# Optimization experiments

Hardware: AMD Instinct MI355X
Metric: run time of the kernel (lower is better)

The kernel has to match this reference:

```python
import jax, jax.numpy as jnp
import numpy as np

IN_FEATURES_LS = (64, 128, 256, 512)
OUT_FEATURES = 1024
MAX_FEAT = max(IN_FEATURES_LS)
N_TOKENS = 65536


def setup_inputs() -> dict:
    key = jax.random.key(0)
    kx, kg, kw, kb = jax.random.split(key, 4)
    x = jax.random.normal(kx, (N_TOKENS, MAX_FEAT), dtype=jnp.float32)
    gidx = jax.random.randint(kg, (N_TOKENS,), 0, len(IN_FEATURES_LS))
    # per-sample declared input size; values are exactly entries of IN_FEATURES_LS
    in_feat_size = jnp.asarray(IN_FEATURES_LS, dtype=jnp.int64 if jax.config.jax_enable_x64 else jnp.int32)[gidx]
    weight = jax.random.normal(kw, (len(IN_FEATURES_LS), OUT_FEATURES, MAX_FEAT), dtype=jnp.float32) * 0.02
    bias = jax.random.normal(kb, (len(IN_FEATURES_LS), OUT_FEATURES), dtype=jnp.float32) * 0.02
    return {"x": x, "in_feat_size": in_feat_size, "weight": weight, "bias": bias}


def reference(x, in_feat_size, weight, bias):
    # mask[g, i] = i < in_features_ls[g]; zero out padded weight columns
    sizes = jnp.asarray(IN_FEATURES_LS, dtype=jnp.int32)
    feat_mask = (jnp.arange(MAX_FEAT)[None, :] < sizes[:, None]).astype(x.dtype)  # [G, max_feat]
    out = jnp.zeros(x.shape[:-1] + (OUT_FEATURES,), dtype=x.dtype)
    for idx, feat_size in enumerate(IN_FEATURES_LS):
        w = weight[idx] * feat_mask[idx][None, :]          # [out, max_feat]
        y = jnp.einsum('oi,ni->no', w, x) + bias[idx]       # [N, out]
        sel = (in_feat_size == feat_size).astype(x.dtype)[..., None]
        out = out + sel * y
    return out
```

## Files before the change

kernel.cpp:

```cpp
#include <hip/hip_runtime.h>
#include <hip/hip_bf16.h>

#define N_TOKENS 65536
#define MAXF 512
#define OUTF 1024
#define NGROUP 4

typedef __attribute__((ext_vector_type(8))) short short8;
typedef __attribute__((ext_vector_type(4))) float floatx4;
typedef unsigned short ushort_t;
typedef unsigned int uint_t;

__device__ __forceinline__ uint_t f2bf(float f) {
    uint_t u = __float_as_uint(f);
    u += 0x7fffu + ((u >> 16) & 1u);
    return u >> 16;
}

#define OFF_BASES  0
#define OFF_BHIST  4096
#define OFF_BSTART 8192
#define OFF_LISTS  16384
#define OFF_XB     (1u<<20)
#define OFF_WB     ((1u<<20) + ((size_t)N_TOKENS*MAXF*2))
#define WS_FULL    (OFF_WB + (size_t)NGROUP*OUTF*MAXF*2)
#define WS_MIN     (OFF_LISTS + (size_t)N_TOKENS*4)

__global__ void hist_kernel(const int* __restrict__ sizes, int* __restrict__ blockHist) {
    __shared__ int h[4][NGROUP];
    int t = threadIdx.x, wave = t >> 6;
    int tok = blockIdx.x * 256 + t;
    int g = __ffs(sizes[tok]) - 7;
    #pragma unroll
    for (int gg = 0; gg < NGROUP; ++gg) {
        unsigned long long m = __ballot(g == gg);
        if ((t & 63) == 0) h[wave][gg] = __popcll(m);
    }
    __syncthreads();
    if (t < NGROUP)
        blockHist[blockIdx.x * NGROUP + t] = h[0][t] + h[1][t] + h[2][t] + h[3][t];
}

__global__ void scan_kernel(const int* __restrict__ blockHist,
                            int* __restrict__ blockStart, int* __restrict__ bases) {
    __shared__ int4 sh[256];
    int t = threadIdx.x;
    int4 v = ((const int4*)blockHist)[t];
    sh[t] = v;
    __syncthreads();
    for (int d = 1; d < 256; d <<= 1) {
        int4 u = sh[t];
        int4 a = make_int4(0, 0, 0, 0);
        if (t >= d) a = sh[t - d];
        __syncthreads();
        u.x += a.x; u.y += a.y; u.z += a.z; u.w += a.w;
        sh[t] = u;
        __syncthreads();
    }
    int4 incl = sh[t];
    int4 tot = sh[255];
    int b0 = 0, b1 = tot.x, b2 = b1 + tot.y, b3 = b2 + tot.z, b4 = b3 + tot.w;
    blockStart[t * 4 + 0] = b0 + incl.x - v.x;
    blockStart[t * 4 + 1] = b1 + incl.y - v.y;
    blockStart[t * 4 + 2] = b2 + incl.z - v.z;
    blockStart[t * 4 + 3] = b3 + incl.w - v.w;
    if (t == 0) {
        bases[0] = b0; bases[1] = b1; bases[2] = b2; bases[3] = b3; bases[4] = b4;
    }
}

__global__ void scatter_kernel(const int* __restrict__ sizes,
                               const int* __restrict__ blockStart,
                               int* __restrict__ lists) {
    __shared__ int wcnt[4][NGROUP];
    int t = threadIdx.x, wave = t >> 6, lane = t & 63;
    int tok = blockIdx.x * 256 + t;
    int g = __ffs(sizes[tok]) - 7;
    int pos = 0;
    #pragma unroll
    for (int gg = 0; gg < NGROUP; ++gg) {
        unsigned long long m = __ballot(g == gg);
        if (g == gg) pos = __popcll(m & ((1ull << lane) - 1ull));
        if (lane == 0) wcnt[wave][gg] = __popcll(m);
    }
    __syncthreads();
    int off = blockStart[blockIdx.x * 4 + g];
    for (int w = 0; w < wave; ++w) off += wcnt[w][g];
    lists[off + pos] = tok;
}

__global__ void convx_kernel(const float* __restrict__ x, const int* __restrict__ bases,
                             const int* __restrict__ lists, ushort_t* __restrict__ xb) {
    int slot = blockIdx.x * 4 + (threadIdx.x >> 6);
    int lane = threadIdx.x & 63;
    int b1 = bases[1], b2 = bases[2], b3 = bases[3];
    int g = (slot >= b3) ? 3 : (slot >= b2) ? 2 : (slot >= b1) ? 1 : 0;
    int K = 64 << g;
    int tok = lists[slot];
    const float2* src = (const float2*)(x + (size_t)tok * MAXF);
    uint_t* dst = (uint_t*)(xb + (size_t)slot * MAXF);
    for (int j = lane; j * 2 < K; j += 64) {
        float2 v = src[j];
        dst[j] = f2bf(v.x) | (f2bf(v.y) << 16);
    }
}

__global__ void convw_kernel(const float* __restrict__ weight, ushort_t* __restrict__ wb) {
    int id = blockIdx.x * 256 + threadIdx.x;
    floatx4 v = ((const floatx4*)weight)[id];
    unsigned long long p = (unsigned long long)f2bf(v[0]) |
                           ((unsigned long long)f2bf(v[1]) << 16) |
                           ((unsigned long long)f2bf(v[2]) << 32) |
                           ((unsigned long long)f2bf(v[3]) << 48);
    ((unsigned long long*)wb)[id] = p;
}

#define GLOAD_LDS16(gptr, lptr)                                                \
    __builtin_amdgcn_global_load_lds(                                          \
        (const __attribute__((address_space(1))) uint_t*)(gptr),               \
        (__attribute__((address_space(3))) uint_t*)(lptr), 16, 0, 0)

__global__ __launch_bounds__(256) void gemm_bf16_kernel(
    const ushort_t* __restrict__ xb, const ushort_t* __restrict__ wb,
    const float* __restrict__ bias, const int* __restrict__ bases,
    const int* __restrict__ lists, float* __restrict__ out) {

    const int g = blockIdx.z;
    const int gbase = bases[g];
    const int count = bases[g + 1] - gbase;
    const int m_base = blockIdx.y * 128;
    if (m_base >= count) return;
    const int n_base = blockIdx.x * 128;
    const int K = 64 << g;
    const int rows = min(128, count - m_base);

    __shared__ ushort_t As[128 * 32];
    __shared__ ushort_t Bs[128 * 32];
    __shared__ int oidx[128];

    const int t = threadIdx.x;
    const int wave = t >> 6, lane = t & 63;
    const int wm = wave >> 1, wn = wave & 1;
    const int quad = lane >> 4, l16 = lane & 15;

    const int rsub = lane >> 2;
    const int ksub = (lane & 3) * 8;

    floatx4 acc[4][4];
    #pragma unroll
    for (int i = 0; i < 4; ++i)
        #pragma unroll
        for (int j = 0; j < 4; ++j) acc[i][j] = (floatx4)(0.0f);

    const ushort_t* wg = wb + (size_t)g * OUTF * MAXF;

    for (int k0 = 0; k0 < K; k0 += 32) {
        #pragma unroll
        for (int j = 0; j < 2; ++j) {
            int br = wave * 32 + j * 16;
            int ga = min(gbase + m_base + br + rsub, N_TOKENS - 1);
            GLOAD_LDS16(xb + (size_t)ga * MAXF + k0 + ksub, &As[br * 32]);
            int gb = n_base + br + rsub;
            GLOAD_LDS16(wg + (size_t)gb * MAXF + k0 + ksub, &Bs[br * 32]);
        }
        __syncthreads();

        short8 af[4], bf[4];
        #pragma unroll
        for (int mi = 0; mi < 4; ++mi)
            af[mi] = *(const short8*)&As[(wm * 64 + mi * 16 + l16) * 32 + quad * 8];
        #pragma unroll
        for (int ni = 0; ni < 4; ++ni)
            bf[ni] = *(const short8*)&Bs[(wn * 64 + ni * 16 + l16) * 32 + quad * 8];

        #pragma unroll
        for (int mi = 0; mi < 4; ++mi)
            #pragma unroll
            for (int ni = 0; ni < 4; ++ni)
                acc[mi][ni] = __builtin_amdgcn_mfma_f32_16x16x32_bf16(
                    af[mi], bf[ni], acc[mi][ni], 0, 0, 0);
        __syncthreads();
    }

    if (t < 128) oidx[t] = (t < rows) ? lists[gbase + m_base + t] : 0;
    __syncthreads();

    #pragma unroll
    for (int ni = 0; ni < 4; ++ni) {
        int col = n_base + wn * 64 + ni * 16 + l16;
        float bv = bias[g * OUTF + col];
        #pragma unroll
        for (int mi = 0; mi < 4; ++mi) {
            int mloc = wm * 64 + mi * 16 + quad * 4;
            #pragma unroll
            for (int r = 0; r < 4; ++r) {
                int m = mloc + r;
                if (m < rows)
                    out[(size_t)oidx[m] * OUTF + col] = acc[mi][ni][r] + bv;
            }
        }
    }
}

__global__ __launch_bounds__(256) void gemm_fp32_kernel(
    const float* __restrict__ x, const float* __restrict__ weight,
    const float* __restrict__ bias, const int* __restrict__ bases,
    const int* __restrict__ lists, float* __restrict__ out) {

    const int g = blockIdx.z;
    const int gbase = bases[g];
    const int count = bases[g + 1] - gbase;
    const int m_base = blockIdx.y * 128;
    if (m_base >= count) return;
    const int n_base = blockIdx.x * 128;
    const int K = 64 << g;
    const int rows = min(128, count - m_base);

    __shared__ ushort_t As[128][40];
    __shared__ ushort_t Bs[128][40];
    __shared__ int idxs[128];

    const int t = threadIdx.x;
    if (t < 128) idxs[t] = (t < rows) ? lists[gbase + m_base + t] : lists[gbase + m_base];
    __syncthreads();

    const int wave = t >> 6, lane = t & 63;
    const int wm = wave >> 1, wn = wave & 1;
    const int quad = lane >> 4, l16 = lane & 15;

    floatx4 acc[4][4];
    #pragma unroll
    for (int i = 0; i < 4; ++i)
        #pragma unroll
        for (int j = 0; j < 4; ++j) acc[i][j] = (floatx4)(0.0f);

    const float* wg = weight + (size_t)g * OUTF * MAXF;

    for (int k0 = 0; k0 < K; k0 += 32) {
        #pragma unroll
        for (int rep = 0; rep < 4; ++rep) {
            int id = t + rep * 256;
            int row = id >> 3;
            int kq = id & 7;
            floatx4 av = *(const floatx4*)(x + (size_t)idxs[row] * MAXF + k0 + kq * 4);
            unsigned long long pa = (unsigned long long)f2bf(av[0]) |
                ((unsigned long long)f2bf(av[1]) << 16) |
                ((unsigned long long)f2bf(av[2]) << 32) |
                ((unsigned long long)f2bf(av[3]) << 48);
            *(unsigned long long*)&As[row][kq * 4] = pa;
            floatx4 bv = *(const floatx4*)(wg + (size_t)(n_base + row) * MAXF + k0 + kq * 4);
            unsigned long long pb = (unsigned long long)f2bf(bv[0]) |
                ((unsigned long long)f2bf(bv[1]) << 16) |
                ((unsigned long long)f2bf(bv[2]) << 32) |
                ((unsigned long long)f2bf(bv[3]) << 48);
            *(unsigned long long*)&Bs[row][kq * 4] = pb;
        }
        __syncthreads();

        short8 af[4], bf[4];
        #pragma unroll
        for (int mi = 0; mi < 4; ++mi)
            af[mi] = *(const short8*)&As[wm * 64 + mi * 16 + l16][quad * 8];
        #pragma unroll
        for (int ni = 0; ni < 4; ++ni)
            bf[ni] = *(const short8*)&Bs[wn * 64 + ni * 16 + l16][quad * 8];
        #pragma unroll
        for (int mi = 0; mi < 4; ++mi)
            #pragma unroll
            for (int ni = 0; ni < 4; ++ni)
                acc[mi][ni] = __builtin_amdgcn_mfma_f32_16x16x32_bf16(
                    af[mi], bf[ni], acc[mi][ni], 0, 0, 0);
        __syncthreads();
    }

    #pragma unroll
    for (int ni = 0; ni < 4; ++ni) {
        int col = n_base + wn * 64 + ni * 16 + l16;
        float bv = bias[g * OUTF + col];
        #pragma unroll
        for (int mi = 0; mi < 4; ++mi) {
            int mloc = wm * 64 + mi * 16 + quad * 4;
            #pragma unroll
            for (int r = 0; r < 4; ++r) {
                int m = mloc + r;
                if (m < rows)
                    out[(size_t)idxs[m] * OUTF + col] = acc[mi][ni][r] + bv;
            }
        }
    }
}

extern "C" void kernel_launch(void* const* d_in, const int* in_sizes, int n_in,
                              void* d_out, int out_size, void* d_ws, size_t ws_size,
                              hipStream_t stream) {
    const float* x      = (const float*)d_in[0];
    const int*   sizes  = (const int*)d_in[1];
    const float* weight = (const float*)d_in[2];
    const float* bias   = (const float*)d_in[3];
    float* out = (float*)d_out;

    char* ws = (char*)d_ws;
    int* bases      = (int*)(ws + OFF_BASES);
    int* blockHist  = (int*)(ws + OFF_BHIST);
    int* blockStart = (int*)(ws + OFF_BSTART);
    int* lists      = (int*)(ws + OFF_LISTS);
    ushort_t* xb    = (ushort_t*)(ws + OFF_XB);
    ushort_t* wb    = (ushort_t*)(ws + OFF_WB);

    hist_kernel<<<N_TOKENS / 256, 256, 0, stream>>>(sizes, blockHist);
    scan_kernel<<<1, 256, 0, stream>>>(blockHist, blockStart, bases);
    scatter_kernel<<<N_TOKENS / 256, 256, 0, stream>>>(sizes, blockStart, lists);

    dim3 grid(OUTF / 128, N_TOKENS / 128, NGROUP);
    if (ws_size >= WS_FULL) {
        convw_kernel<<<(NGROUP * OUTF * MAXF / 4) / 256, 256, 0, stream>>>(weight, wb);
        convx_kernel<<<N_TOKENS / 4, 256, 0, stream>>>(x, bases, lists, xb);
        gemm_bf16_kernel<<<grid, 256, 0, stream>>>(xb, wb, bias, bases, lists, out);
    } else {
        gemm_fp32_kernel<<<grid, 256, 0, stream>>>(x, weight, bias, bases, lists, out);
    }
}
```

Baseline: 488.1 us.

## Pack bf16 operands compactly, use 256x256 double-buffered tiles and flat grid

Converted x and weights are now stored densely with a per-group row stride equal to K instead of MAXF, and the conversion kernels use 8-element vectors with grid-stride loops. The GEMM moves to 512-thread blocks with 256x256 tiles, double-buffered LDS prefetch and a flattened 1D grid that only launches the tiles each group needs. The intent is to cut memory traffic, raise operand reuse, overlap loads with MFMA work and drop the empty blocks from the old 3D grid. In exchange the kernel uses more registers and LDS, bases[4] is read where the old code did not, and the grid size of 1036 is hardcoded.

Result: no change. 484.5 us (-0.7%).

```diff
diff --git a/kernel.cpp b/kernel.cpp
--- a/kernel.cpp
+++ b/kernel.cpp
@@ -25,6 +25,8 @@
 #define OFF_WB     ((1u<<20) + ((size_t)N_TOKENS*MAXF*2))
 #define WS_FULL    (OFF_WB + (size_t)NGROUP*OUTF*MAXF*2)
 #define WS_MIN     (OFF_LISTS + (size_t)N_TOKENS*4)
+
+__constant__ int c_wstart[4] = {0, 65536, 196608, 458752};
 
 __global__ void hist_kernel(const int* __restrict__ sizes, int* __restrict__ blockHist) {
     __shared__ int h[4][NGROUP];
@@ -91,28 +93,55 @@
 
 __global__ void convx_kernel(const float* __restrict__ x, const int* __restrict__ bases,
                              const int* __restrict__ lists, ushort_t* __restrict__ xb) {
-    int slot = blockIdx.x * 4 + (threadIdx.x >> 6);
-    int lane = threadIdx.x & 63;
-    int b1 = bases[1], b2 = bases[2], b3 = bases[3];
-    int g = (slot >= b3) ? 3 : (slot >= b2) ? 2 : (slot >= b1) ? 1 : 0;
-    int K = 64 << g;
-    int tok = lists[slot];
-    const float2* src = (const float2*)(x + (size_t)tok * MAXF);
-    uint_t* dst = (uint_t*)(xb + (size_t)slot * MAXF);
-    for (int j = lane; j * 2 < K; j += 64) {
-        float2 v = src[j];
-        dst[j] = f2bf(v.x) | (f2bf(v.y) << 16);
+    int c0 = bases[1] - bases[0], c1 = bases[2] - bases[1],
+        c2 = bases[3] - bases[2], c3 = bases[4] - bases[3];
+    int p1 = c0 << 3;
+    int p2 = p1 + (c1 << 4);
+    int p3 = p2 + (c2 << 5);
+    int T  = p3 + (c3 << 6);
+    int xs1 = c0 << 6;
+    int xs2 = xs1 + (c1 << 7);
+    int xs3 = xs2 + (c2 << 8);
+    int stride = gridDim.x * blockDim.x;
+    for (int id = blockIdx.x * blockDim.x + threadIdx.x; id < T; id += stride) {
+        int g, local, base, xs;
+        if (id < p1)      { g = 0; local = id;      base = bases[0]; xs = 0;   }
+        else if (id < p2) { g = 1; local = id - p1; base = bases[1]; xs = xs1; }
+        else if (id < p3) { g = 2; local = id - p2; base = bases[2]; xs = xs2; }
+        else              { g = 3; local = id - p3; base = bases[3]; xs = xs3; }
+        int shift = 3 + g;
+        int sl = local >> shift;
+        int k  = (local - (sl << shift)) << 3;
+        int tok = lists[base + sl];
+        const floatx4* src = (const floatx4*)(x + (size_t)tok * MAXF + k);
+        floatx4 a = src[0], b = src[1];
+        short8 v;
+        v[0] = (short)f2bf(a[0]); v[1] = (short)f2bf(a[1]);
+        v[2] = (short)f2bf(a[2]); v[3] = (short)f2bf(a[3]);
+        v[4] = (short)f2bf(b[0]); v[5] = (short)f2bf(b[1]);
+        v[6] = (short)f2bf(b[2]); v[7] = (short)f2bf(b[3]);
+        *(short8*)(xb + (size_t)xs + ((size_t)sl << (6 + g)) + k) = v;
     }
 }
 
 __global__ void convw_kernel(const float* __restrict__ weight, ushort_t* __restrict__ wb) {
     int id = blockIdx.x * 256 + threadIdx.x;
-    floatx4 v = ((const floatx4*)weight)[id];
-    unsigned long long p = (unsigned long long)f2bf(v[0]) |
-                           ((unsigned long long)f2bf(v[1]) << 16) |
-                           ((unsigned long long)f2bf(v[2]) << 32) |
-                           ((unsigned long long)f2bf(v[3]) << 48);
-    ((unsigned long long*)wb)[id] = p;
+    int g, local, ws;
+    if (id < 8192)       { g = 0; local = id;         ws = 0;      }
+    else if (id < 24576) { g = 1; local = id - 8192;  ws = 65536;  }
+    else if (id < 57344) { g = 2; local = id - 24576; ws = 196608; }
+    else                 { g = 3; local = id - 57344; ws = 458752; }
+    int shift = 3 + g;
+    int row = local >> shift;
+    int k = (local - (row << shift)) << 3;
+    const floatx4* src = (const floatx4*)(weight + (size_t)g * OUTF * MAXF + (size_t)row * MAXF + k);
+    floatx4 a = src[0], b = src[1];
+    short8 v;
+    v[0] = (short)f2bf(a[0]); v[1] = (short)f2bf(a[1]);
+    v[2] = (short)f2bf(a[2]); v[3] = (short)f2bf(a[3]);
+    v[4] = (short)f2bf(b[0]); v[5] = (short)f2bf(b[1]);
+    v[6] = (short)f2bf(b[2]); v[7] = (short)f2bf(b[3]);
+    *(short8*)(wb + ws + ((size_t)row << (6 + g)) + k) = v;
 }
 
 #define GLOAD_LDS16(gptr, lptr)                                                \
@@ -120,8 +149,121 @@
         (const __attribute__((address_space(1))) uint_t*)(gptr),               \
         (__attribute__((address_space(3))) uint_t*)(lptr), 16, 0, 0)
 
-__global__ __launch_bounds__(256) void gemm_bf16_kernel(
+__global__ __launch_bounds__(512, 1) void gemm_bf16_kernel(
     const ushort_t* __restrict__ xb, const ushort_t* __restrict__ wb,
+    const float* __restrict__ bias, const int* __restrict__ bases,
+    const int* __restrict__ lists, float* __restrict__ out) {
+
+    const int c0 = bases[1] - bases[0], c1 = bases[2] - bases[1],
+              c2 = bases[3] - bases[2], c3 = bases[4] - bases[3];
+    const int t0 = ((c0 + 255) >> 8) << 2;
+    const int t1 = ((c1 + 255) >> 8) << 2;
+    const int t2 = ((c2 + 255) >> 8) << 2;
+    const int t3 = ((c3 + 255) >> 8) << 2;
+    const int xs1 = c0 << 6;
+    const int xs2 = xs1 + (c1 << 7);
+    const int xs3 = xs2 + (c2 << 8);
+
+    int id = blockIdx.x;
+    int g, local, count, gbase, xs, wsb;
+    if (id < t0)                { g = 0; local = id;                count = c0; gbase = bases[0]; xs = 0;   wsb = 0;      }
+    else if (id < t0 + t1)      { g = 1; local = id - t0;           count = c1; gbase = bases[1]; xs = xs1; wsb = 65536;  }
+    else if (id < t0 + t1 + t2) { g = 2; local = id - t0 - t1;      count = c2; gbase = bases[2]; xs = xs2; wsb = 196608; }
+    else if (id < t0 + t1 + t2 + t3)
+                                { g = 3; local = id - t0 - t1 - t2; count = c3; gbase = bases[3]; xs = xs3; wsb = 458752; }
+    else return;
+
+    const int mt = local >> 2, nt = local & 3;
+    const int m_base = mt << 8;
+    const int n_base = nt << 8;
+    const int K_log = 6 + g;
+    const int nsteps = 1 << (g + 1);
+    const int rows = min(256, count - m_base);
+
+    __shared__ ushort_t As[2][256 * 32];
+    __shared__ ushort_t Bs[2][256 * 32];
+
+    const int t = threadIdx.x;
+    const int wave = t >> 6, lane = t & 63;
+    const int wm = wave >> 2, wn = wave & 3;
+    const int quad = lane >> 4, l16 = lane & 15;
+    const int rsub = lane >> 2;
+    const int kq   = (lane & 3) * 8;
+
+    const ushort_t* aptr[2];
+    const ushort_t* bptr[2];
+    #pragma unroll
+    for (int j = 0; j < 2; ++j) {
+        int br = wave * 32 + j * 16;
+        int ar = min(m_base + br + rsub, count - 1);
+        aptr[j] = xb + (size_t)xs + ((size_t)ar << K_log) + kq;
+        int nr = n_base + br + rsub;
+        bptr[j] = wb + (size_t)wsb + ((size_t)nr << K_log) + kq;
+    }
+
+    floatx4 acc[8][4];
+    #pragma unroll
+    for (int i = 0; i < 8; ++i)
+        #pragma unroll
+        for (int j = 0; j < 4; ++j) acc[i][j] = (floatx4)(0.0f);
+
+    #pragma unroll
+    for (int j = 0; j < 2; ++j) {
+        int br = wave * 32 + j * 16;
+        GLOAD_LDS16(aptr[j], &As[0][br * 32]);
+        GLOAD_LDS16(bptr[j], &Bs[0][br * 32]);
+    }
+    __syncthreads();
+
+    int buf = 0;
+    for (int s = 0; s < nsteps; ++s) {
+        if (s + 1 < nsteps) {
+            int k0 = (s + 1) << 5;
+            #pragma unroll
+            for (int j = 0; j < 2; ++j) {
+                int br = wave * 32 + j * 16;
+                GLOAD_LDS16(aptr[j] + k0, &As[buf ^ 1][br * 32]);
+                GLOAD_LDS16(bptr[j] + k0, &Bs[buf ^ 1][br * 32]);
+            }
+        }
+        short8 af[8], bf[4];
+        #pragma unroll
+        for (int mi = 0; mi < 8; ++mi)
+            af[mi] = *(const short8*)&As[buf][(wm * 128 + mi * 16 + l16) * 32 + quad * 8];
+        #pragma unroll
+        for (int ni = 0; ni < 4; ++ni)
+            bf[ni] = *(const short8*)&Bs[buf][(wn * 64 + ni * 16 + l16) * 32 + quad * 8];
+        #pragma unroll
+        for (int mi = 0; mi < 8; ++mi)
+            #pragma unroll
+            for (int ni = 0; ni < 4; ++ni)
+                acc[mi][ni] = __builtin_amdgcn_mfma_f32_16x16x32_bf16(
+                    af[mi], bf[ni], acc[mi][ni], 0, 0, 0);
+        __syncthreads();
+        buf ^= 1;
+    }
+
+    #pragma unroll
+    for (int ni = 0; ni < 4; ++ni) {
+        int col = n_base + wn * 64 + ni * 16 + l16;
+        float bv = bias[g * OUTF + col];
+        #pragma unroll
+        for (int mi = 0; mi < 8; ++mi) {
+            int mloc = wm * 128 + mi * 16 + quad * 4;
+            #pragma unroll
+            for (int r = 0; r < 4; ++r) {
+                int m = mloc + r;
+                if (m < rows) {
+                    int tok = lists[gbase + m_base + m];
+                    out[(size_t)tok * OUTF + col] = acc[mi][ni][r] + bv;
+                }
+            }
+        }
+    }
+}
+
+__global__ __launch_bounds__(256) void gemm_fp32_kernel(
+    const float* __restrict__ x, const float* __restrict__ weight,
     const float* __restrict__ bias, const int* __restrict__ bases,
     const int* __restrict__ lists, float* __restrict__ out) {
 
@@ -134,100 +276,18 @@
     const int K = 64 << g;
     const int rows = min(128, count - m_base);
 
-    __shared__ ushort_t As[128 * 32];
-    __shared__ ushort_t Bs[128 * 32];
-    __shared__ int oidx[128];
+    __shared__ ushort_t As[128][40];
+    __shared__ ushort_t Bs[128][40];
+    __shared__ int idxs[128];
 
     const int t = threadIdx.x;
+    if (t < 128) idxs[t] = (t < rows) ? lists[gbase + m_base + t] : lists[gbase + m_base];
+    __syncthreads();
+
     const int wave = t >> 6, lane = t & 63;
     const int wm = wave >> 1, wn = wave & 1;
     const int quad = lane >> 4, l16 = lane & 15;
 
-    const int rsub = lane >> 2;
-    const int ksub = (lane & 3) * 8;
-
-    floatx4 acc[4][4];
-    #pragma unroll
-    for (int i = 0; i < 4; ++i)
-        #pragma unroll
-        for (int j = 0; j < 4; ++j) acc[i][j] = (floatx4)(0.0f);
-
-    const ushort_t* wg = wb + (size_t)g * OUTF * MAXF;
-
-    for (int k0 = 0; k0 < K; k0 += 32) {
-        #pragma unroll
-        for (int j = 0; j < 2; ++j) {
-            int br = wave * 32 + j * 16;
-            int ga = min(gbase + m_base + br + rsub, N_TOKENS - 1);
-            GLOAD_LDS16(xb + (size_t)ga * MAXF + k0 + ksub, &As[br * 32]);
-            int gb = n_base + br + rsub;
-            GLOAD_LDS16(wg + (size_t)gb * MAXF + k0 + ksub, &Bs[br * 32]);
-        }
-        __syncthreads();
-
-        short8 af[4], bf[4];
-        #pragma unroll
-        for (int mi = 0; mi < 4; ++mi)
-            af[mi] = *(const short8*)&As[(wm * 64 + mi * 16 + l16) * 32 + quad * 8];
-        #pragma unroll
-        for (int ni = 0; ni < 4; ++ni)
-            bf[ni] = *(const short8*)&Bs[(wn * 64 + ni * 16 + l16) * 32 + quad * 8];
-
-        #pragma unroll
-        for (int mi = 0; mi < 4; ++mi)
-            #pragma unroll
-            for (int ni = 0; ni < 4; ++ni)
-                acc[mi][ni] = __builtin_amdgcn_mfma_f32_16x16x32_bf16(
-                    af[mi], bf[ni], acc[mi][ni], 0, 0, 0);
-        __syncthreads();
-    }
-
-    if (t < 128) oidx[t] = (t < rows) ? lists[gbase + m_base + t] : 0;
-    __syncthreads();
-
-    #pragma unroll
-    for (int ni = 0; ni < 4; ++ni) {
-        int col = n_base + wn * 64 + ni * 16 + l16;
-        float bv = bias[g * OUTF + col];
-        #pragma unroll
-        for (int mi = 0; mi < 4; ++mi) {
-            int mloc = wm * 64 + mi * 16 + quad * 4;
-            #pragma unroll
-            for (int r = 0; r < 4; ++r) {
-                int m = mloc + r;
-                if (m < rows)
-                    out[(size_t)oidx[m] * OUTF + col] = acc[mi][ni][r] + bv;
-            }
-        }
-    }
-}
-
-__global__ __launch_bounds__(256) void gemm_fp32_kernel(
-    const float* __restrict__ x, const float* __restrict__ weight,
-    const float* __restrict__ bias, const int* __restrict__ bases,
-    const int* __restrict__ lists, float* __restrict__ out) {
-
-    const int g = blockIdx.z;
-    const int gbase = bases[g];
-    const int count = bases[g + 1] - gbase;
-    const int m_base = blockIdx.y * 128;
-    if (m_base >= count) return;
-    const int n_base = blockIdx.x * 128;
-    const int K = 64 << g;
-    const int rows = min(128, count - m_base);
-
-    __shared__ ushort_t As[128][40];
-    __shared__ ushort_t Bs[128][40];
-    __shared__ int idxs[128];
-
-    const int t = threadIdx.x;
-    if (t < 128) idxs[t] = (t < rows) ? lists[gbase + m_base + t] : lists[gbase + m_base];
-    __syncthreads();
-
-    const int wave = t >> 6, lane = t & 63;
-    const int wm = wave >> 1, wn = wave & 1;
-    const int quad = lane >> 4, l16 = lane & 15;
-
     floatx4 acc[4][4];
     #pragma unroll
     for (int i = 0; i < 4; ++i)
@@ -241,19 +301,19 @@
         for (int rep = 0; rep < 4; ++rep) {
             int id = t + rep * 256;
             int row = id >> 3;
-            int kq = id & 7;
-            floatx4 av = *(const floatx4*)(x + (size_t)idxs[row] * MAXF + k0 + kq * 4);
+            int kqq = id & 7;
+            floatx4 av = *(const floatx4*)(x + (size_t)idxs[row] * MAXF + k0 + kqq * 4);
             unsigned long long pa = (unsigned long long)f2bf(av[0]) |
                 ((unsigned long long)f2bf(av[1]) << 16) |
                 ((unsigned long long)f2bf(av[2]) << 32) |
                 ((unsigned long long)f2bf(av[3]) << 48);
-            *(unsigned long long*)&As[row][kq * 4] = pa;
-            floatx4 bv = *(const floatx4*)(wg + (size_t)(n_base + row) * MAXF + k0 + kq * 4);
-            unsigned long long pb = (unsigned long long)f2bf(bv[0]) |
-                ((unsigned long long)f2bf(bv[1]) << 16) |
-                ((unsigned long long)f2bf(bv[2]) << 32) |
-                ((unsigned long long)f2bf(bv[3]) << 48);
-            *(unsigned long long*)&Bs[row][kq * 4] = pb;
+            *(unsigned long long*)&As[row][kqq * 4] = pa;
+            floatx4 bvv = *(const floatx4*)(wg + (size_t)(n_base + row) * MAXF + k0 + kqq * 4);
+            unsigned long long pb = (unsigned long long)f2bf(bvv[0]) |
+                ((unsigned long long)f2bf(bvv[1]) << 16) |
+                ((unsigned long long)f2bf(bvv[2]) << 32) |
+                ((unsigned long long)f2bf(bvv[3]) << 48);
+            *(unsigned long long*)&Bs[row][kqq * 4] = pb;
         }
         __syncthreads();
 
@@ -311,12 +371,12 @@
     scan_kernel<<<1, 256, 0, stream>>>(blockHist, blockStart, bases);
     scatter_kernel<<<N_TOKENS / 256, 256, 0, stream>>>(sizes, blockStart, lists);
 
-    dim3 grid(OUTF / 128, N_TOKENS / 128, NGROUP);
     if (ws_size >= WS_FULL) {
-        convw_kernel<<<(NGROUP * OUTF * MAXF / 4) / 256, 256, 0, stream>>>(weight, wb);
-        convx_kernel<<<N_TOKENS / 4, 256, 0, stream>>>(x, bases, lists, xb);
-        gemm_bf16_kernel<<<grid, 256, 0, stream>>>(xb, wb, bias, bases, lists, out);
+        convw_kernel<<<480, 256, 0, stream>>>(weight, wb);
+        convx_kernel<<<2048, 256, 0, stream>>>(x, bases, lists, xb);
+        gemm_bf16_kernel<<<1036, 512, 0, stream>>>(xb, wb, bias, bases, lists, out);
     } else {
+        dim3 grid(OUTF / 128, N_TOKENS / 128, NGROUP);
         gemm_fp32_kernel<<<grid, 256, 0, stream>>>(x, weight, bias, bases, lists, out);
     }
 }
```
